# Performance work log

Measured on AMD Instinct MI355X. Metric: run time of the kernel, lower is better.

Reference implementation:

```python
import jax, jax.numpy as jnp
import numpy as np

N_NODES = 100_000
E_OFF = 1_000_000
HID = 32
GF = 8
NF = 8
N_LAYERS = 3


def _mlp(h, W1, b1, W2, b2):
    # Linear -> ReLU -> Linear (matches MLP([in, hidden, out]))
    return jax.nn.relu(h @ W1 + b1) @ W2 + b2


def _seg_mean(v, idx, n):
    s = jax.ops.segment_sum(v, idx, num_segments=n)
    c = jax.ops.segment_sum(jnp.ones((v.shape[0], 1), v.dtype), idx, num_segments=n)
    return s / jnp.maximum(c, 1.0)


def _graphnet(x, row, col, eattr2, g, p):
    # GraphNet with global block: edge MLP -> mean-aggregate to nodes -> node MLP -> global MLP
    eW1, eb1, eW2, eb2, nW1, nb1, nW2, nb2, gW1, gb1, gW2, gb2 = p
    n, e = x.shape[0], row.shape[0]
    gE = jnp.broadcast_to(g, (e, g.shape[1]))
    e_emb = _mlp(jnp.concatenate([gE, x[row], x[col], eattr2], axis=1), eW1, eb1, eW2, eb2)
    agg = _seg_mean(e_emb, row, n)
    gN = jnp.broadcast_to(g, (n, g.shape[1]))
    n_emb = _mlp(jnp.concatenate([gN, x, agg], axis=1), nW1, nb1, nW2, nb2)
    g_new = _mlp(jnp.concatenate([n_emb.mean(0, keepdims=True), e_emb.mean(0, keepdims=True), g], axis=1),
                 gW1, gb1, gW2, gb2)
    return e_emb, n_emb, g_new


def setup_inputs() -> dict:
    key = jax.random.key(0)
    ks = jax.random.split(key, 24)
    a = jax.random.randint(ks[0], (E_OFF,), 0, N_NODES)
    b = jax.random.randint(ks[1], (E_OFF,), 0, N_NODES)
    d = jnp.arange(N_NODES)
    l_ei = jnp.stack([jnp.concatenate([jnp.maximum(a, b), d]),
                      jnp.concatenate([jnp.minimum(a, b), d])])  # lower triangular + diag
    c = jax.random.randint(ks[2], (E_OFF,), 0, N_NODES)
    e = jax.random.randint(ks[3], (E_OFF,), 0, N_NODES)
    u_ei = jnp.stack([jnp.concatenate([jnp.minimum(c, e), d]),
                      jnp.concatenate([jnp.maximum(c, e), d])])  # upper triangular + diag
    E = E_OFF + N_NODES
    x = jax.random.normal(ks[4], (N_NODES, NF), dtype=jnp.float32)
    l_attr = jax.random.normal(ks[5], (E, 1), dtype=jnp.float32)
    u_attr = jax.random.normal(ks[6], (E, 1), dtype=jnp.float32)

    def w(k, shape):
        return (jax.random.normal(k, shape, dtype=jnp.float32) / np.sqrt(shape[-2])).astype(jnp.float32)

    e_in = GF + 2 * NF + 1 + 1  # 26 (edge attr padded to 2: skip col, zeros where absent)
    n_in = GF + 1 + NF          # 17
    g_in = NF + 1 + GF          # 17
    return {
        'x': x, 'l_edge_index': l_ei, 'u_edge_index': u_ei,
        'l_edge_attr': l_attr, 'u_edge_attr': u_attr,
        'eW1': w(ks[7], (2, N_LAYERS, e_in, HID)), 'eb1': 0.01 * jax.random.normal(ks[8], (2, N_LAYERS, HID)),
        'eW2': w(ks[9], (2, N_LAYERS, HID, 1)), 'eb2': 0.01 * jax.random.normal(ks[10], (2, N_LAYERS, 1)),
        'nW1': w(ks[11], (2, N_LAYERS, n_in, HID)), 'nb1': 0.01 * jax.random.normal(ks[12], (2, N_LAYERS, HID)),
        'nW2': w(ks[13], (2, N_LAYERS, HID, NF)), 'nb2': 0.01 * jax.random.normal(ks[14], (2, N_LAYERS, NF)),
        'gW1': w(ks[15], (2, N_LAYERS, g_in, HID)), 'gb1': 0.01 * jax.random.normal(ks[16], (2, N_LAYERS, HID)),
        'gW2': w(ks[17], (2, N_LAYERS, HID, GF)), 'gb2': 0.01 * jax.random.normal(ks[18], (2, N_LAYERS, GF)),
    }


def reference(x, l_edge_index, u_edge_index, l_edge_attr, u_edge_attr,
              eW1, eb1, eW2, eb2, nW1, nb1, nW2, nb2, gW1, gb1, gW2, gb2):
    params = (eW1, eb1, eW2, eb2, nW1, nb1, nW2, nb2, gW1, gb1, gW2, gb2)
    lr, lc = l_edge_index[0], l_edge_index[1]
    ur, uc = u_edge_index[0], u_edge_index[1]
    g = jnp.zeros((1, GF), x.dtype)
    l_e, u_e = l_edge_attr, u_edge_attr
    l_a = l_edge_attr  # skip-connection edge features (original matrix values)
    zl, zu = jnp.zeros_like(l_edge_attr), jnp.zeros_like(u_edge_attr)
    for i in range(N_LAYERS):
        p1 = tuple(w[0, i] for w in params)
        p2 = tuple(w[1, i] for w in params)
        l_in = jnp.concatenate([l_e, l_a if i != 0 else zl], axis=1)  # zeros col == no skip (block 0)
        l_e, l_n, g = _graphnet(x, lr, lc, l_in, g, p1)
        u_in = jnp.concatenate([u_e, zu], axis=1)  # l2 never has skip; padded zeros col
        u_e, u_n, g = _graphnet(l_n, ur, uc, u_in, g, p2)
        # NOTE: node embeddings are NOT carried across MP blocks in the original
    l_vals = jnp.where(lr == lc, jnp.exp(l_e[:, 0]), l_e[:, 0])
    u_vals = jnp.where(ur == uc, jnp.exp(u_e[:, 0]), u_e[:, 0])
    return jnp.concatenate([l_vals, u_vals])
```

## Files before the change

### kernel.cpp

```cpp
#include <hip/hip_runtime.h>


typedef unsigned int u32;

#define NB_SHIFT 9
#define NB_SIZE 512
#define RSTRIDE 1104

__device__ __forceinline__ float wave_sum(float v) {
#pragma unroll
    for (int off = 32; off > 0; off >>= 1) v += __shfl_down(v, off, 64);
    return v;
}


__global__ __launch_bounds__(256) void hist_kernel(
    const int* __restrict__ lr, const int* __restrict__ ur,
    u32* __restrict__ hist, int E, int B) {
    __shared__ u32 h[256];
    const int t = threadIdx.x;
    if (t < B) h[t] = 0;
    __syncthreads();
    const int s = blockIdx.y;
    const int* rows = s ? ur : lr;
    for (int i = blockIdx.x * 256 + t; i < E; i += gridDim.x * 256)
        atomicAdd(&h[rows[i] >> NB_SHIFT], 1u);
    __syncthreads();
    if (t < B && h[t]) atomicAdd(&hist[s * B + t], h[t]);
}

__global__ __launch_bounds__(256) void scan_kernel(
    const u32* __restrict__ hist, u32* __restrict__ offs,
    u32* __restrict__ cur, int B) {
    __shared__ u32 sh[256];
    const int t = threadIdx.x;
    for (int s = 0; s < 2; ++s) {
        const u32 v = (t < B) ? hist[s * B + t] : 0u;
        sh[t] = v;
        __syncthreads();
#pragma unroll
        for (int off = 1; off < 256; off <<= 1) {
            const u32 add = (t >= off) ? sh[t - off] : 0u;
            __syncthreads();
            sh[t] += add;
            __syncthreads();
        }
        const u32 exc = sh[t] - v;
        if (t < B) {
            offs[s * (B + 1) + t] = exc;
            cur[s * B + t] = exc;
        }
        if (t == 255) offs[s * (B + 1) + B] = sh[255];
        __syncthreads();
    }
}

#define SCHUNK 4096
__global__ __launch_bounds__(256) void scatter_kernel(
    const int* __restrict__ lr, const int* __restrict__ ur,
    const int* __restrict__ lc, const int* __restrict__ uc,
    const float* __restrict__ la, const float* __restrict__ ua,
    u32* __restrict__ cur, u32* __restrict__ list,
    int* __restrict__ rs, int* __restrict__ cs, float* __restrict__ as_,
    int E, int B) {
    __shared__ u32 lcnt[256], lbase[256];
    const int t = threadIdx.x;
    const int s = blockIdx.y;
    const int* rows = s ? ur : lr;
    const int* cols = s ? uc : lc;
    const float* attr = s ? ua : la;
    u32* mylist = list + (size_t)s * E;
    int* myrs = rs + (size_t)s * E;
    int* mycs = cs + (size_t)s * E;
    float* myas = as_ + (size_t)s * E;
    if (t < B) lcnt[t] = 0;
    __syncthreads();
    const int base_e = blockIdx.x * SCHUNK;
#pragma unroll
    for (int k = 0; k < SCHUNK / 256; ++k) {
        const int e = base_e + k * 256 + t;
        if (e < E) atomicAdd(&lcnt[rows[e] >> NB_SHIFT], 1u);
    }
    __syncthreads();
    if (t < B) {
        const u32 c = lcnt[t];
        lbase[t] = c ? atomicAdd(&cur[s * B + t], c) : 0u;
        lcnt[t] = 0;
    }
    __syncthreads();
#pragma unroll
    for (int k = 0; k < SCHUNK / 256; ++k) {
        const int e = base_e + k * 256 + t;
        if (e < E) {
            const int rv = rows[e];
            const int b = rv >> NB_SHIFT;
            const u32 pos = lbase[b] + atomicAdd(&lcnt[b], 1u);
            mylist[pos] = (u32)e;
            myrs[pos] = rv;
            mycs[pos] = cols[e];
            myas[pos] = attr[e];
        }
    }
}


template <bool SKIP, bool GAGG, bool VALS, bool STORE, bool GCOMP>
__global__ __launch_bounds__(256, 3) void edge_kernel(
    const float4* __restrict__ xf,
    const int* __restrict__ rows, const int* __restrict__ cols,
    const float* __restrict__ eprev,
    const float* __restrict__ skipattr,
    const u32* __restrict__ ids,
    const float* __restrict__ W1,
    const float* __restrict__ b1,
    const float* __restrict__ W2,
    const float* __restrict__ b2,
    const float* __restrict__ gprev,
    float* __restrict__ gout,
    const float* __restrict__ pebins,
    const float* __restrict__ pnbins,
    const float* __restrict__ gW1, const float* __restrict__ gb1,
    const float* __restrict__ gW2, const float* __restrict__ gb2,
    float* __restrict__ ebins,
    float* __restrict__ e_out,
    float* __restrict__ vals_out,
    int E, int N, float inv_E) {
    __shared__ float gsh[8];
    __shared__ float biasE[32];
    __shared__ float wpart[4];
    const int t = threadIdx.x;
    if constexpr (GCOMP) {
        if (t < 64) {
            float nb[8];
#pragma unroll
            for (int q = 0; q < 8; ++q) nb[q] = pnbins[t * 16 + q];
            const float eb = pebins[t];
            float gin[17];
#pragma unroll
            for (int q = 0; q < 8; ++q) {
                const float s = wave_sum(nb[q]);
                gin[q] = __shfl(s, 0, 64) / (float)N;
            }
            const float es = wave_sum(eb);
            gin[8] = __shfl(es, 0, 64) * inv_E;
#pragma unroll
            for (int k = 0; k < 8; ++k) gin[9 + k] = gprev[k];
            float hv = 0.0f;
            if (t < 32) {
                hv = gb1[t];
#pragma unroll
                for (int k = 0; k < 17; ++k)
                    hv = fmaf(gin[k], gW1[k * 32 + t], hv);
                hv = fmaxf(hv, 0.0f);
            }
#pragma unroll
            for (int q = 0; q < 8; ++q) {
                const float c = (t < 32) ? hv * gW2[t * 8 + q] : 0.0f;
                const float s = wave_sum(c);
                if (t == 0) {
                    const float gv = gb2[q] + s;
                    gsh[q] = gv;
                    if (blockIdx.x == 0) gout[q] = gv;
                }
            }
        }
    } else {
        if (t < 8) gsh[t] = gprev[t];
    }
    __syncthreads();
    if (t < 32) {
        float v = b1[t];
#pragma unroll
        for (int k = 0; k < 8; ++k) v = fmaf(gsh[k], W1[k * 32 + t], v);
        biasE[t] = v;
    }
    __syncthreads();

    const int e = blockIdx.x * 256 + t;
    const bool valid = e < E;
    const int idx = valid ? e : 0;
    const int r = rows[idx];
    const int c = cols[idx];
    const float4 xr0 = xf[2 * r], xr1 = xf[2 * r + 1];
    const float4 xc0 = xf[2 * c], xc1 = xf[2 * c + 1];
    float in[18] = {xr0.x, xr0.y, xr0.z, xr0.w, xr1.x, xr1.y, xr1.z, xr1.w,
                    xc0.x, xc0.y, xc0.z, xc0.w, xc1.x, xc1.y, xc1.z, xc1.w,
                    eprev[idx], 0.0f};
    if constexpr (SKIP) in[17] = skipattr[idx];

    float h[32];
#pragma unroll
    for (int q = 0; q < 8; ++q) {
        const float4 b = reinterpret_cast<const float4*>(biasE)[q];
        h[4 * q + 0] = b.x; h[4 * q + 1] = b.y;
        h[4 * q + 2] = b.z; h[4 * q + 3] = b.w;
    }
    const float4* __restrict__ W4 =
        reinterpret_cast<const float4*>(W1 + 8 * 32);
#pragma unroll
    for (int k = 0; k < 18; ++k) {
        const float v = in[k];
#pragma unroll
        for (int q = 0; q < 8; ++q) {
            const float4 w = W4[k * 8 + q];
            h[4 * q + 0] = fmaf(v, w.x, h[4 * q + 0]);
            h[4 * q + 1] = fmaf(v, w.y, h[4 * q + 1]);
            h[4 * q + 2] = fmaf(v, w.z, h[4 * q + 2]);
            h[4 * q + 3] = fmaf(v, w.w, h[4 * q + 3]);
        }
    }
    float out = b2[0];
    const float4* __restrict__ W24 = reinterpret_cast<const float4*>(W2);
#pragma unroll
    for (int q = 0; q < 8; ++q) {
        const float4 w = W24[q];
        out = fmaf(fmaxf(h[4 * q + 0], 0.f), w.x, out);
        out = fmaf(fmaxf(h[4 * q + 1], 0.f), w.y, out);
        out = fmaf(fmaxf(h[4 * q + 2], 0.f), w.z, out);
        out = fmaf(fmaxf(h[4 * q + 3], 0.f), w.w, out);
    }

    if (valid) {
        if constexpr (STORE) e_out[e] = out;
        if constexpr (VALS) vals_out[ids[e]] = (r == c) ? expf(out) : out;
    }
    if constexpr (GAGG) {
        const float s = wave_sum(valid ? out : 0.0f);
        if ((t & 63) == 0) wpart[t >> 6] = s;
        __syncthreads();
        if (t == 0)
            atomicAdd(&ebins[blockIdx.x & 63],
                      wpart[0] + wpart[1] + wpart[2] + wpart[3]);
    }
}


template <bool COUNT, bool STORE_N>
__global__ __launch_bounds__(1024) void aggnode_kernel(
    const u32* __restrict__ offs,
    const int* __restrict__ rows,
    const float* __restrict__ e_emb,
    const float4* __restrict__ xf,
    float* __restrict__ cntf,
    const float* __restrict__ g,
    const float* __restrict__ nW1, const float* __restrict__ nb1,
    const float* __restrict__ nW2, const float* __restrict__ nb2,
    float* __restrict__ n_out,
    float* __restrict__ nbins,
    int N) {
    __shared__ float sbin[NB_SIZE];
    __shared__ float cbin[NB_SIZE];
    __shared__ float biasN[32];
    __shared__ float npart[8][8];
    const int t = threadIdx.x;
    if (t < NB_SIZE) {
        sbin[t] = 0.0f;
        if constexpr (COUNT) cbin[t] = 0.0f;
    }
    if (t >= NB_SIZE && t < NB_SIZE + 32) {
        const int j = t - NB_SIZE;
        float v = nb1[j];
#pragma unroll
        for (int k = 0; k < 8; ++k) v = fmaf(g[k], nW1[k * 32 + j], v);
        biasN[j] = v;
    }
    __syncthreads();
    const int b = blockIdx.x;
    const u32 beg = offs[b], end = offs[b + 1];
    for (u32 i = beg + t; i < end; i += 1024) {
        const float v = e_emb[i];
        const int r = rows[i];
        atomicAdd(&sbin[r & (NB_SIZE - 1)], v);
        if constexpr (COUNT) atomicAdd(&cbin[r & (NB_SIZE - 1)], 1.0f);
    }
    __syncthreads();

    const int n0 = b << NB_SHIFT;
    float o[8];
    const bool active = (t < NB_SIZE) && (n0 + t < N);
    if (t < NB_SIZE) {
        const int n = n0 + t;
        const int idx = active ? n : (N - 1);
        float cntv;
        if constexpr (COUNT) {
            cntv = cbin[t];
            if (active) cntf[n] = cntv;
        } else {
            cntv = cntf[idx];
        }
        const float agg = sbin[t] / fmaxf(cntv, 1.0f);
        const float4 x0 = xf[2 * idx], x1 = xf[2 * idx + 1];
        float in[9] = {x0.x, x0.y, x0.z, x0.w, x1.x, x1.y, x1.z, x1.w, agg};
        float h[32];
#pragma unroll
        for (int j = 0; j < 8; ++j) {
            const float4 bb = reinterpret_cast<const float4*>(biasN)[j];
            h[4 * j + 0] = bb.x; h[4 * j + 1] = bb.y;
            h[4 * j + 2] = bb.z; h[4 * j + 3] = bb.w;
        }
        const float* __restrict__ Wk = nW1 + 8 * 32;
#pragma unroll
        for (int k = 0; k < 9; ++k) {
            const float v = in[k];
#pragma unroll
            for (int j = 0; j < 32; ++j) h[j] = fmaf(v, Wk[k * 32 + j], h[j]);
        }
#pragma unroll
        for (int q = 0; q < 8; ++q) o[q] = nb2[q];
#pragma unroll
        for (int j = 0; j < 32; ++j) {
            const float hv = fmaxf(h[j], 0.0f);
#pragma unroll
            for (int q = 0; q < 8; ++q) o[q] = fmaf(hv, nW2[j * 8 + q], o[q]);
        }
        if constexpr (STORE_N) {
            if (active) {
                reinterpret_cast<float4*>(n_out)[2 * n] =
                    make_float4(o[0], o[1], o[2], o[3]);
                reinterpret_cast<float4*>(n_out)[2 * n + 1] =
                    make_float4(o[4], o[5], o[6], o[7]);
            }
        }
#pragma unroll
        for (int q = 0; q < 8; ++q) {
            const float s = wave_sum(active ? o[q] : 0.0f);
            if ((t & 63) == 0) npart[t >> 6][q] = s;
        }
    }
    __syncthreads();
    if (t < 8) {
        float a = 0.0f;
#pragma unroll
        for (int w = 0; w < 8; ++w) a += npart[w][t];
        atomicAdd(&nbins[(b & 63) * 16 + t], a);
    }
}

extern "C" void kernel_launch(void* const* d_in, const int* in_sizes, int n_in,
                              void* d_out, int out_size, void* d_ws,
                              size_t ws_size, hipStream_t stream) {
    const float* x = (const float*)d_in[0];
    const int* l_ei = (const int*)d_in[1];
    const int* u_ei = (const int*)d_in[2];
    const float* l_attr = (const float*)d_in[3];
    const float* u_attr = (const float*)d_in[4];
    const float* eW1 = (const float*)d_in[5];
    const float* eb1 = (const float*)d_in[6];
    const float* eW2 = (const float*)d_in[7];
    const float* eb2 = (const float*)d_in[8];
    const float* nW1 = (const float*)d_in[9];
    const float* nb1 = (const float*)d_in[10];
    const float* nW2 = (const float*)d_in[11];
    const float* nb2 = (const float*)d_in[12];
    const float* gW1 = (const float*)d_in[13];
    const float* gb1 = (const float*)d_in[14];
    const float* gW2 = (const float*)d_in[15];
    const float* gb2 = (const float*)d_in[16];

    const int E = in_sizes[3];
    const int N = in_sizes[0] / 8;
    const int B = (N + NB_SIZE - 1) >> NB_SHIFT;

    float* ws = (float*)d_ws;
    float* l_e = ws;
    float* u_e = l_e + E;
    float* l_n = u_e + E;
    float* cnt_l = l_n + (size_t)8 * N;
    float* cnt_u = cnt_l + N;
    float* gslot = cnt_u + N;
    u32* hist = (u32*)(gslot + 56);
    float* dyn_all = (float*)(hist + 2 * B);
    u32* offs = (u32*)(dyn_all + 5 * RSTRIDE);
    u32* cur = offs + 2 * (B + 1);
    u32* list = cur + 2 * B;
    int* rs = (int*)(list + (size_t)2 * E);
    int* cs = rs + (size_t)2 * E;
    float* as_ = (float*)(cs + (size_t)2 * E);

    const int* lr = l_ei;
    const int* lc = l_ei + E;
    const int* ur = u_ei;
    const int* uc = u_ei + E;
    const int eg = (E + 255) / 256;
    const int sg = (E + SCHUNK - 1) / SCHUNK;
    const float invE = 1.0f / (float)E;
    float* outL = (float*)d_out;
    float* outU = outL + E;
    const u32* offs_l = offs;
    const u32* offs_u = offs + (B + 1);

    hipMemsetAsync(gslot, 0, (size_t)(56 + 2 * B + 5 * RSTRIDE) * sizeof(float),
                   stream);
    hist_kernel<<<dim3(128, 2), 256, 0, stream>>>(lr, ur, hist, E, B);
    scan_kernel<<<1, 256, 0, stream>>>(hist, offs, cur, B);
    scatter_kernel<<<dim3(sg, 2), 256, 0, stream>>>(lr, ur, lc, uc, l_attr,
                                                    u_attr, cur, list, rs, cs,
                                                    as_, E, B);

    const size_t wsl[6] = {0, 3, 1, 4, 2, 5};

    for (int j = 0; j < 6; ++j) {
        const bool lower = !(j & 1);
        const size_t sl = wsl[j];
        float* ebins = dyn_all + (size_t)(j <= 4 ? j : 4) * RSTRIDE;
        float* nbins = ebins + 64;
        const float* pe = (j >= 1) ? dyn_all + (size_t)(j - 1) * RSTRIDE : nullptr;
        const float* pn = (j >= 1) ? pe + 64 : nullptr;
        const size_t psl = (j >= 1) ? wsl[j - 1] : 0;
        const float4* exf = (const float4*)(lower ? x : l_n);
        const int* rows_s = lower ? rs : rs + E;
        const int* cols_s = lower ? cs : cs + E;
        const float* attr_s = lower ? as_ : as_ + E;
        const u32* ids = lower ? list : list + E;
        const float* eprev = (j <= 1) ? attr_s : (lower ? l_e : u_e);
        float* e_out = lower ? l_e : u_e;
        const float* gprev = gslot + (size_t)(j >= 1 ? j - 1 : 0) * 8;
        float* gout = gslot + (size_t)j * 8;

#define EDGE_ARGS                                                             \
    exf, rows_s, cols_s, eprev, attr_s, ids, eW1 + sl * 832, eb1 + sl * 32,   \
        eW2 + sl * 32, eb2 + sl, gprev, gout, pe, pn, gW1 + psl * 544,        \
        gb1 + psl * 32, gW2 + psl * 256, gb2 + psl * 8, ebins, e_out,         \
        (j == 4) ? outL : outU, E, N, invE

        switch (j) {
            case 0: edge_kernel<false, true, false, true, false>
                        <<<eg, 256, 0, stream>>>(EDGE_ARGS); break;
            case 1: edge_kernel<false, true, false, true, true>
                        <<<eg, 256, 0, stream>>>(EDGE_ARGS); break;
            case 2: edge_kernel<true, true, false, true, true>
                        <<<eg, 256, 0, stream>>>(EDGE_ARGS); break;
            case 3: edge_kernel<false, true, false, true, true>
                        <<<eg, 256, 0, stream>>>(EDGE_ARGS); break;
            case 4: edge_kernel<true, true, true, true, true>
                        <<<eg, 256, 0, stream>>>(EDGE_ARGS); break;
            case 5: edge_kernel<false, false, true, false, true>
                        <<<eg, 256, 0, stream>>>(EDGE_ARGS); break;
        }
#undef EDGE_ARGS

        if (j == 5) break;

        const u32* aoffs = lower ? offs_l : offs_u;
        float* cntf = lower ? cnt_l : cnt_u;
        const float4* nxf = (const float4*)(lower ? x : l_n);

#define AGG_ARGS                                                              \
    aoffs, rows_s, e_out, nxf, cntf, gslot + (size_t)j * 8, nW1 + sl * 544,   \
        nb1 + sl * 32, nW2 + sl * 256, nb2 + sl * 8, l_n, nbins, N

        switch (j) {
            case 0: aggnode_kernel<true, true>
                        <<<B, 1024, 0, stream>>>(AGG_ARGS); break;
            case 1: aggnode_kernel<true, false>
                        <<<B, 1024, 0, stream>>>(AGG_ARGS); break;
            case 2: aggnode_kernel<false, true>
                        <<<B, 1024, 0, stream>>>(AGG_ARGS); break;
            case 3: aggnode_kernel<false, false>
                        <<<B, 1024, 0, stream>>>(AGG_ARGS); break;
            case 4: aggnode_kernel<false, true>
                        <<<B, 1024, 0, stream>>>(AGG_ARGS); break;
        }
#undef AGG_ARGS
    }
}
```

Baseline: 569.1 us.

## Pack sorted edge records into int4 and defer output unpermutation to gather pass

The scatter pass now writes one packed int4 record per sorted edge (row, col, attr) plus an inverse permutation, instead of four separate arrays. Edge outputs are stored as float2 pairs holding the value and the local row bin, so the aggregation kernel reads a single float2 instead of separate embedding and row arrays. The final-layer values are written in sorted order and a new unperm kernel gathers them into original order, replacing scattered stores inside the edge kernel. This trades fewer separate streams and coalesced writes for wider records (extra padding bytes) and an added gather kernel launch.

```diff
diff --git a/kernel.cpp b/kernel.cpp
--- a/kernel.cpp
+++ b/kernel.cpp
@@ -60,8 +60,7 @@
     const int* __restrict__ lr, const int* __restrict__ ur,
     const int* __restrict__ lc, const int* __restrict__ uc,
     const float* __restrict__ la, const float* __restrict__ ua,
-    u32* __restrict__ cur, u32* __restrict__ list,
-    int* __restrict__ rs, int* __restrict__ cs, float* __restrict__ as_,
+    u32* __restrict__ cur, int4* __restrict__ pk, u32* __restrict__ inv,
     int E, int B) {
     __shared__ u32 lcnt[256], lbase[256];
     const int t = threadIdx.x;
@@ -69,10 +68,8 @@
     const int* rows = s ? ur : lr;
     const int* cols = s ? uc : lc;
     const float* attr = s ? ua : la;
-    u32* mylist = list + (size_t)s * E;
-    int* myrs = rs + (size_t)s * E;
-    int* mycs = cs + (size_t)s * E;
-    float* myas = as_ + (size_t)s * E;
+    int4* mypk = pk + (size_t)s * E;
+    u32* myinv = inv + (size_t)s * E;
     if (t < B) lcnt[t] = 0;
     __syncthreads();
     const int base_e = blockIdx.x * SCHUNK;
@@ -95,22 +92,18 @@
             const int rv = rows[e];
             const int b = rv >> NB_SHIFT;
             const u32 pos = lbase[b] + atomicAdd(&lcnt[b], 1u);
-            mylist[pos] = (u32)e;
-            myrs[pos] = rv;
-            mycs[pos] = cols[e];
-            myas[pos] = attr[e];
-        }
-    }
-}
-
-
-template <bool SKIP, bool GAGG, bool VALS, bool STORE, bool GCOMP>
+            mypk[pos] = make_int4(rv, cols[e], __float_as_int(attr[e]), 0);
+            myinv[e] = pos;
+        }
+    }
+}
+
+
+template <bool SKIP, bool GAGG, bool VALS, bool STORE, bool GCOMP, bool EPF2>
 __global__ __launch_bounds__(256, 3) void edge_kernel(
     const float4* __restrict__ xf,
-    const int* __restrict__ rows, const int* __restrict__ cols,
-    const float* __restrict__ eprev,
-    const float* __restrict__ skipattr,
-    const u32* __restrict__ ids,
+    const int4* __restrict__ pk,
+    const float2* __restrict__ eprevf2,
     const float* __restrict__ W1,
     const float* __restrict__ b1,
     const float* __restrict__ W2,
@@ -122,8 +115,8 @@
     const float* __restrict__ gW1, const float* __restrict__ gb1,
     const float* __restrict__ gW2, const float* __restrict__ gb2,
     float* __restrict__ ebins,
-    float* __restrict__ e_out,
-    float* __restrict__ vals_out,
+    float2* __restrict__ e_out,
+    float* __restrict__ vsort,
     int E, int N, float inv_E) {
     __shared__ float gsh[8];
     __shared__ float biasE[32];
@@ -179,14 +172,19 @@
     const int e = blockIdx.x * 256 + t;
     const bool valid = e < E;
     const int idx = valid ? e : 0;
-    const int r = rows[idx];
-    const int c = cols[idx];
+    const int4 p = pk[idx];
+    const int r = p.x;
+    const int c = p.y;
+    const float attr = __int_as_float(p.z);
+    float epv;
+    if constexpr (EPF2) epv = eprevf2[idx].x;
+    else epv = attr;
     const float4 xr0 = xf[2 * r], xr1 = xf[2 * r + 1];
     const float4 xc0 = xf[2 * c], xc1 = xf[2 * c + 1];
     float in[18] = {xr0.x, xr0.y, xr0.z, xr0.w, xr1.x, xr1.y, xr1.z, xr1.w,
                     xc0.x, xc0.y, xc0.z, xc0.w, xc1.x, xc1.y, xc1.z, xc1.w,
-                    eprev[idx], 0.0f};
-    if constexpr (SKIP) in[17] = skipattr[idx];
+                    epv, 0.0f};
+    if constexpr (SKIP) in[17] = attr;
 
     float h[32];
 #pragma unroll
@@ -221,8 +219,9 @@
     }
 
     if (valid) {
-        if constexpr (STORE) e_out[e] = out;
-        if constexpr (VALS) vals_out[ids[e]] = (r == c) ? expf(out) : out;
+        if constexpr (STORE)
+            e_out[e] = make_float2(out, __int_as_float(r & (NB_SIZE - 1)));
+        if constexpr (VALS) vsort[e] = (r == c) ? expf(out) : out;
     }
     if constexpr (GAGG) {
         const float s = wave_sum(valid ? out : 0.0f);
@@ -238,8 +237,7 @@
 template <bool COUNT, bool STORE_N>
 __global__ __launch_bounds__(1024) void aggnode_kernel(
     const u32* __restrict__ offs,
-    const int* __restrict__ rows,
-    const float* __restrict__ e_emb,
+    const float2* __restrict__ em,
     const float4* __restrict__ xf,
     float* __restrict__ cntf,
     const float* __restrict__ g,
@@ -268,10 +266,10 @@
     const int b = blockIdx.x;
     const u32 beg = offs[b], end = offs[b + 1];
     for (u32 i = beg + t; i < end; i += 1024) {
-        const float v = e_emb[i];
-        const int r = rows[i];
-        atomicAdd(&sbin[r & (NB_SIZE - 1)], v);
-        if constexpr (COUNT) atomicAdd(&cbin[r & (NB_SIZE - 1)], 1.0f);
+        const float2 v = em[i];
+        const int rl = __float_as_int(v.y);
+        atomicAdd(&sbin[rl], v.x);
+        if constexpr (COUNT) atomicAdd(&cbin[rl], 1.0f);
     }
     __syncthreads();
 
@@ -333,6 +331,18 @@
 #pragma unroll
         for (int w = 0; w < 8; ++w) a += npart[w][t];
         atomicAdd(&nbins[(b & 63) * 16 + t], a);
+    }
+}
+
+
+__global__ __launch_bounds__(256) void unperm_kernel(
+    const float* __restrict__ vs,
+    const u32* __restrict__ inv,
+    float* __restrict__ out, int E) {
+    const int i = blockIdx.x * 256 + threadIdx.x;
+    if (i < 2 * E) {
+        const u32 p = inv[i];
+        out[i] = (i < E) ? vs[p] : vs[E + p];
     }
 }
 
@@ -362,9 +372,12 @@
     const int B = (N + NB_SIZE - 1) >> NB_SHIFT;
 
     float* ws = (float*)d_ws;
-    float* l_e = ws;
-    float* u_e = l_e + E;
-    float* l_n = u_e + E;
+    int4* pk = (int4*)ws;
+    float* l_e = ws + (size_t)8 * E;
+    float* u_e = l_e + (size_t)2 * E;
+    float* vs = u_e + (size_t)2 * E;
+    u32* inv = (u32*)(vs + (size_t)2 * E);
+    float* l_n = (float*)(inv + (size_t)2 * E);
     float* cnt_l = l_n + (size_t)8 * N;
     float* cnt_u = cnt_l + N;
     float* gslot = cnt_u + N;
@@ -372,10 +385,6 @@
     float* dyn_all = (float*)(hist + 2 * B);
     u32* offs = (u32*)(dyn_all + 5 * RSTRIDE);
     u32* cur = offs + 2 * (B + 1);
-    u32* list = cur + 2 * B;
-    int* rs = (int*)(list + (size_t)2 * E);
-    int* cs = rs + (size_t)2 * E;
-    float* as_ = (float*)(cs + (size_t)2 * E);
 
     const int* lr = l_ei;
     const int* lc = l_ei + E;
@@ -384,8 +393,7 @@
     const int eg = (E + 255) / 256;
     const int sg = (E + SCHUNK - 1) / SCHUNK;
     const float invE = 1.0f / (float)E;
-    float* outL = (float*)d_out;
-    float* outU = outL + E;
+    float* outAll = (float*)d_out;
     const u32* offs_l = offs;
     const u32* offs_u = offs + (B + 1);
 
@@ -394,8 +402,7 @@
     hist_kernel<<<dim3(128, 2), 256, 0, stream>>>(lr, ur, hist, E, B);
     scan_kernel<<<1, 256, 0, stream>>>(hist, offs, cur, B);
     scatter_kernel<<<dim3(sg, 2), 256, 0, stream>>>(lr, ur, lc, uc, l_attr,
-                                                    u_attr, cur, list, rs, cs,
-                                                    as_, E, B);
+                                                    u_attr, cur, pk, inv, E, B);
 
     const size_t wsl[6] = {0, 3, 1, 4, 2, 5};
 
@@ -408,33 +415,31 @@
         const float* pn = (j >= 1) ? pe + 64 : nullptr;
         const size_t psl = (j >= 1) ? wsl[j - 1] : 0;
         const float4* exf = (const float4*)(lower ? x : l_n);
-        const int* rows_s = lower ? rs : rs + E;
-        const int* cols_s = lower ? cs : cs + E;
-        const float* attr_s = lower ? as_ : as_ + E;
-        const u32* ids = lower ? list : list + E;
-        const float* eprev = (j <= 1) ? attr_s : (lower ? l_e : u_e);
-        float* e_out = lower ? l_e : u_e;
+        const int4* pks = lower ? pk : pk + E;
+        const float2* eprevf2 =
+            (const float2*)(lower ? l_e : u_e);
+        float2* e_out = (float2*)(lower ? l_e : u_e);
+        float* vsort = lower ? vs : vs + E;
         const float* gprev = gslot + (size_t)(j >= 1 ? j - 1 : 0) * 8;
         float* gout = gslot + (size_t)j * 8;
 
 #define EDGE_ARGS                                                             \
-    exf, rows_s, cols_s, eprev, attr_s, ids, eW1 + sl * 832, eb1 + sl * 32,   \
-        eW2 + sl * 32, eb2 + sl, gprev, gout, pe, pn, gW1 + psl * 544,        \
-        gb1 + psl * 32, gW2 + psl * 256, gb2 + psl * 8, ebins, e_out,         \
-        (j == 4) ? outL : outU, E, N, invE
+    exf, pks, eprevf2, eW1 + sl * 832, eb1 + sl * 32, eW2 + sl * 32,          \
+        eb2 + sl, gprev, gout, pe, pn, gW1 + psl * 544, gb1 + psl * 32,       \
+        gW2 + psl * 256, gb2 + psl * 8, ebins, e_out, vsort, E, N, invE
 
         switch (j) {
-            case 0: edge_kernel<false, true, false, true, false>
-                        <<<eg, 256, 0, stream>>>(EDGE_ARGS); break;
-            case 1: edge_kernel<false, true, false, true, true>
-                        <<<eg, 256, 0, stream>>>(EDGE_ARGS); break;
-            case 2: edge_kernel<true, true, false, true, true>
-                        <<<eg, 256, 0, stream>>>(EDGE_ARGS); break;
-            case 3: edge_kernel<false, true, false, true, true>
-                        <<<eg, 256, 0, stream>>>(EDGE_ARGS); break;
-            case 4: edge_kernel<true, true, true, true, true>
-                        <<<eg, 256, 0, stream>>>(EDGE_ARGS); break;
-            case 5: edge_kernel<false, false, true, false, true>
+            case 0: edge_kernel<false, true, false, true, false, false>
+                        <<<eg, 256, 0, stream>>>(EDGE_ARGS); break;
+            case 1: edge_kernel<false, true, false, true, true, false>
+                        <<<eg, 256, 0, stream>>>(EDGE_ARGS); break;
+            case 2: edge_kernel<true, true, false, true, true, true>
+                        <<<eg, 256, 0, stream>>>(EDGE_ARGS); break;
+            case 3: edge_kernel<false, true, false, true, true, true>
+                        <<<eg, 256, 0, stream>>>(EDGE_ARGS); break;
+            case 4: edge_kernel<true, true, true, true, true, true>
+                        <<<eg, 256, 0, stream>>>(EDGE_ARGS); break;
+            case 5: edge_kernel<false, false, true, false, true, true>
                         <<<eg, 256, 0, stream>>>(EDGE_ARGS); break;
         }
 #undef EDGE_ARGS
@@ -444,9 +449,10 @@
         const u32* aoffs = lower ? offs_l : offs_u;
         float* cntf = lower ? cnt_l : cnt_u;
         const float4* nxf = (const float4*)(lower ? x : l_n);
+        const float2* em = (const float2*)(lower ? l_e : u_e);
 
 #define AGG_ARGS                                                              \
-    aoffs, rows_s, e_out, nxf, cntf, gslot + (size_t)j * 8, nW1 + sl * 544,   \
+    aoffs, em, nxf, cntf, gslot + (size_t)j * 8, nW1 + sl * 544,              \
         nb1 + sl * 32, nW2 + sl * 256, nb2 + sl * 8, l_n, nbins, N
 
         switch (j) {
@@ -463,4 +469,6 @@
         }
 #undef AGG_ARGS
     }
-}
+
+    unperm_kernel<<<(2 * E + 255) / 256, 256, 0, stream>>>(vs, inv, outAll, E);
+}
```

New measurement: 550.3 us. 3.3% less time.
